# Kernel tuning notes

Hardware: AMD Instinct MI355X
Metric: run time of the kernel (lower is better)

## Reference

```python
import jax, jax.numpy as jnp
from jax import lax
import numpy as np

B, T, V, H = 512, 512, 96, 128


def setup_inputs() -> dict:
    key = jax.random.key(0)
    ks = jax.random.split(key, 8)
    # one-hot character inputs [B, T, V]
    idx = jax.random.randint(ks[0], (B, T), 0, V)
    x = jax.nn.one_hot(idx, V, dtype=jnp.float32)
    s_ih = 1.0 / np.sqrt(H)  # PyTorch nn.RNN init: U(-1/sqrt(H), 1/sqrt(H))
    W_ih = jax.random.uniform(ks[1], (H, V), jnp.float32, -s_ih, s_ih)
    b_ih = jax.random.uniform(ks[2], (H,), jnp.float32, -s_ih, s_ih)
    W_hh = jax.random.uniform(ks[3], (H, H), jnp.float32, -s_ih, s_ih)
    b_hh = jax.random.uniform(ks[4], (H,), jnp.float32, -s_ih, s_ih)
    s_fc = 1.0 / np.sqrt(H)
    W_fc = jax.random.uniform(ks[5], (V, H), jnp.float32, -s_fc, s_fc)
    b_fc = jax.random.uniform(ks[6], (V,), jnp.float32, -s_fc, s_fc)
    return {"x": x, "W_ih": W_ih, "b_ih": b_ih, "W_hh": W_hh,
            "b_hh": b_hh, "W_fc": W_fc, "b_fc": b_fc}


def reference(x, W_ih, b_ih, W_hh, b_hh, W_fc, b_fc):
    # Precompute input projection for all timesteps (batched GEMM):
    # for one-hot x this is effectively an embedding row gather.
    xW = jnp.einsum('btv,hv->bth', x, W_ih) + b_ih  # [B, T, H]

    def step(h, xt):  # h: [B, H], xt: [B, H]
        h_new = jnp.tanh(xt + h @ W_hh.T + b_hh)
        return h_new, None

    h0 = jnp.zeros((x.shape[0], W_hh.shape[0]), x.dtype)
    hT, _ = lax.scan(step, h0, jnp.swapaxes(xW, 0, 1))  # scan over T
    # fc on the last hidden state only
    return hT @ W_fc.T + b_fc  # [B, V]
```

## Files before the change

### kernel.cpp

```cpp
#include <hip/hip_runtime.h>

#define B_ 512
#define T_ 512
#define V_ 96
#define H_ 128
#define K2F 2.8853900817779268f

typedef _Float16 half8 __attribute__((ext_vector_type(8)));
typedef float    f32x4 __attribute__((ext_vector_type(4)));

__global__ __launch_bounds__(256) void onehot_idx_kernel(
    const float4* __restrict__ x4, int n4, int* __restrict__ idx)
{
    int stride = gridDim.x * blockDim.x;
    for (int e4 = blockIdx.x * blockDim.x + threadIdx.x; e4 < n4; e4 += stride) {
        float4 v = x4[e4];
        int base = e4 * 4;
        if (v.x > 0.5f) idx[(base + 0) / V_] = (base + 0) % V_;
        if (v.y > 0.5f) idx[(base + 1) / V_] = (base + 1) % V_;
        if (v.z > 0.5f) idx[(base + 2) / V_] = (base + 2) % V_;
        if (v.w > 0.5f) idx[(base + 3) / V_] = (base + 3) % V_;
    }
}

__global__ __launch_bounds__(256) void build_xwg_kernel(
    const float* __restrict__ W_ih, const float* __restrict__ b_ih,
    const float* __restrict__ b_hh, float* __restrict__ xwg)
{
    int e = blockIdx.x * 256 + threadIdx.x;
    if (e < V_ * H_) {
        int v = e >> 7, u = e & 127;
        xwg[e] = (W_ih[u * V_ + v] + b_ih[u] + b_hh[u]) * K2F;
    }
}

__global__ __launch_bounds__(256) void build_wB_kernel(
    const float* __restrict__ W_hh, _Float16* __restrict__ wB)
{
    int e = blockIdx.x * 256 + threadIdx.x;
    if (e < 16384) {
        int reg = e & 7, lane = (e >> 3) & 63, mt = (e >> 9) & 7, ks = e >> 12;
        int kin = ks * 32 + (lane >> 4) * 8 + reg;
        int m   = mt * 16 + (lane & 15);
        wB[e] = (_Float16)(K2F * W_hh[m * H_ + kin]);
    }
}

__global__ __launch_bounds__(256) void build_wBfc_kernel(
    const float* __restrict__ W_fc, _Float16* __restrict__ wBfc)
{
    int e = blockIdx.x * 256 + threadIdx.x;
    if (e < 12288) {
        int reg = e & 7, lane = (e >> 3) & 63;
        int mt = (e >> 9) % 6, ks = e / 3072;
        int kin = ks * 32 + (lane >> 4) * 8 + reg;
        int m   = mt * 16 + (lane & 15);
        wBfc[e] = (_Float16)W_fc[m * H_ + kin];
    }
}

__global__ __launch_bounds__(256, 1) void rnn_mfma4_kernel(
    const uint4* __restrict__ wBg, const uint4* __restrict__ wBfcg,
    const float* __restrict__ xwg, const int* __restrict__ idx,
    const float* __restrict__ b_fc, float* __restrict__ out)
{
    const int bb  = blockIdx.x;
    const int tid = threadIdx.x;
    const int w   = tid >> 6;
    const int l   = tid & 63;
    const int lo  = l & 15, g = l >> 4;

    __shared__ _Float16      hs[2][16][136];
    __shared__ unsigned char idxT[(T_ + 1) * 16];

    for (int e = tid; e < 16 * T_; e += 256) {
        int row = e >> 9, t = e & 511;
        idxT[t * 16 + row] = (unsigned char)idx[(bb * 16 + row) * T_ + t];
    }
    if (tid < 16) idxT[T_ * 16 + tid] = 0;
    for (int e = tid; e < 16 * 136; e += 256)
        hs[0][e / 136][e % 136] = (_Float16)0.f;

    uint4 wa[4][2];
    #pragma unroll
    for (int ks = 0; ks < 4; ++ks)
        #pragma unroll
        for (int q = 0; q < 2; ++q)
            wa[ks][q] = wBg[(ks * 8 + 2 * w + q) * 64 + l];

    __syncthreads();

    int id0 = idxT[0 * 16 + lo];
    float4 xcA = *(const float4*)(xwg + id0 * H_ + 32 * w + 4 * g);
    float4 xcB = *(const float4*)(xwg + id0 * H_ + 32 * w + 16 + 4 * g);

    int cur = 0;
    #pragma clang loop unroll(disable)
    for (int t = 0; t < T_; ++t) {
        const int idn = idxT[(t + 1) * 16 + lo];
        const float4 xnA = *(const float4*)(xwg + idn * H_ + 32 * w + 4 * g);
        const float4 xnB = *(const float4*)(xwg + idn * H_ + 32 * w + 16 + 4 * g);

        half8 bF[4];
        #pragma unroll
        for (int ks = 0; ks < 4; ++ks)
            __builtin_memcpy(&bF[ks], &hs[cur][lo][ks * 32 + g * 8], 16);

        f32x4 p0 = {xcA.x, xcA.y, xcA.z, xcA.w};
        f32x4 p1 = {xcB.x, xcB.y, xcB.z, xcB.w};
        f32x4 q0 = {0.f, 0.f, 0.f, 0.f}, q1 = {0.f, 0.f, 0.f, 0.f};
        #pragma unroll
        for (int ks = 0; ks < 2; ++ks) {
            union { uint4 u; half8 h; } u0, u1, u2, u3;
            u0.u = wa[ks][0];     u1.u = wa[ks][1];
            u2.u = wa[ks + 2][0]; u3.u = wa[ks + 2][1];
            p0 = __builtin_amdgcn_mfma_f32_16x16x32_f16(u0.h, bF[ks],     p0, 0, 0, 0);
            p1 = __builtin_amdgcn_mfma_f32_16x16x32_f16(u1.h, bF[ks],     p1, 0, 0, 0);
            q0 = __builtin_amdgcn_mfma_f32_16x16x32_f16(u2.h, bF[ks + 2], q0, 0, 0, 0);
            q1 = __builtin_amdgcn_mfma_f32_16x16x32_f16(u3.h, bF[ks + 2], q1, 0, 0, 0);
        }
        f32x4 acc0 = p0 + q0, acc1 = p1 + q1;

        _Float16 o0[4], o1[4];
        #pragma unroll
        for (int j = 0; j < 4; ++j) {
            float E0 = __builtin_amdgcn_exp2f(acc0[j]);
            float E1 = __builtin_amdgcn_exp2f(acc1[j]);
            o0[j] = (_Float16)(1.0f - 2.0f * __builtin_amdgcn_rcpf(E0 + 1.0f));
            o1[j] = (_Float16)(1.0f - 2.0f * __builtin_amdgcn_rcpf(E1 + 1.0f));
        }
        __builtin_memcpy(&hs[cur ^ 1][lo][32 * w + 4 * g], o0, 8);
        __builtin_memcpy(&hs[cur ^ 1][lo][32 * w + 16 + 4 * g], o1, 8);
        cur ^= 1;

        asm volatile("s_waitcnt lgkmcnt(0)" ::: "memory");
        __builtin_amdgcn_s_barrier();
        __builtin_amdgcn_sched_barrier(0);

        xcA = xnA; xcB = xnB;
    }

    half8 bE[4];
    #pragma unroll
    for (int ks = 0; ks < 4; ++ks)
        __builtin_memcpy(&bE[ks], &hs[0][lo][ks * 32 + g * 8], 16);
    #pragma unroll
    for (int q = 0; q < 2; ++q) {
        const int MT = 2 * w + q;
        if (MT < 6) {
            f32x4 acc;
            __builtin_memcpy(&acc, &b_fc[MT * 16 + 4 * g], 16);
            #pragma unroll
            for (int ks = 0; ks < 4; ++ks) {
                union { uint4 u; half8 h; } ua;
                ua.u = wBfcg[(ks * 6 + MT) * 64 + l];
                acc = __builtin_amdgcn_mfma_f32_16x16x32_f16(ua.h, bE[ks], acc, 0, 0, 0);
            }
            __builtin_memcpy(&out[(bb * 16 + lo) * V_ + MT * 16 + 4 * g], &acc, 16);
        }
    }
}

extern "C" void kernel_launch(void* const* d_in, const int* in_sizes, int n_in,
                              void* d_out, int out_size, void* d_ws, size_t ws_size,
                              hipStream_t stream)
{
    const float* x    = (const float*)d_in[0];
    const float* W_ih = (const float*)d_in[1];
    const float* b_ih = (const float*)d_in[2];
    const float* W_hh = (const float*)d_in[3];
    const float* b_hh = (const float*)d_in[4];
    const float* W_fc = (const float*)d_in[5];
    const float* b_fc = (const float*)d_in[6];
    float* out = (float*)d_out;

    char* ws = (char*)d_ws;
    int*      idx  = (int*)ws;
    float*    xwg  = (float*)(ws + (size_t)B_ * T_ * 4);
    _Float16* wB   = (_Float16*)((char*)xwg + V_ * H_ * 4);
    _Float16* wBfc = (_Float16*)((char*)wB + 16384 * 2);

    const int n4 = (B_ * T_ * V_) / 4;
    hipLaunchKernelGGL(onehot_idx_kernel, dim3(2048), dim3(256), 0, stream,
                       (const float4*)x, n4, idx);
    hipLaunchKernelGGL(build_xwg_kernel, dim3((V_ * H_ + 255) / 256), dim3(256),
                       0, stream, W_ih, b_ih, b_hh, xwg);
    hipLaunchKernelGGL(build_wB_kernel, dim3(64), dim3(256), 0, stream, W_hh, wB);
    hipLaunchKernelGGL(build_wBfc_kernel, dim3(48), dim3(256), 0, stream, W_fc, wBfc);
    hipLaunchKernelGGL(rnn_mfma4_kernel, dim3(B_ / 16), dim3(256), 0, stream,
                       (const uint4*)wB, (const uint4*)wBfc, xwg, idx, b_fc, out);
}
```

Measured before the change: 219.8 us.

## Fold input projection into recurrent MFMA via one-hot LDS operand

Drops the precomputed fp32 xW gather table. The input weights and both biases become three extra K-slices of the fp16 recurrent weight matrix. Each step keeps a one-hot row per sequence in a double-buffered LDS array and multiplies it with MFMA, so the per-step global gather of the input projection goes away. The cost is six extra MFMAs per wave per step, a serial one-hot update by 16 threads before the barrier, and fp16 rounding of the input term.

```diff
diff --git a/kernel.cpp b/kernel.cpp
--- a/kernel.cpp
+++ b/kernel.cpp
@@ -4,6 +4,8 @@
 #define T_ 512
 #define V_ 96
 #define H_ 128
+#define NKS 7
+#define OXP 104
 #define K2F 2.8853900817779268f
 
 typedef _Float16 half8 __attribute__((ext_vector_type(8)));
@@ -23,26 +25,23 @@
     }
 }
 
-__global__ __launch_bounds__(256) void build_xwg_kernel(
-    const float* __restrict__ W_ih, const float* __restrict__ b_ih,
-    const float* __restrict__ b_hh, float* __restrict__ xwg)
+__global__ __launch_bounds__(256) void build_wB_kernel(
+    const float* __restrict__ W_hh, const float* __restrict__ W_ih,
+    const float* __restrict__ b_ih, const float* __restrict__ b_hh,
+    _Float16* __restrict__ wB)
 {
     int e = blockIdx.x * 256 + threadIdx.x;
-    if (e < V_ * H_) {
-        int v = e >> 7, u = e & 127;
-        xwg[e] = (W_ih[u * V_ + v] + b_ih[u] + b_hh[u]) * K2F;
-    }
-}
-
-__global__ __launch_bounds__(256) void build_wB_kernel(
-    const float* __restrict__ W_hh, _Float16* __restrict__ wB)
-{
-    int e = blockIdx.x * 256 + threadIdx.x;
-    if (e < 16384) {
+    if (e < NKS * 8 * 64 * 8) {
         int reg = e & 7, lane = (e >> 3) & 63, mt = (e >> 9) & 7, ks = e >> 12;
-        int kin = ks * 32 + (lane >> 4) * 8 + reg;
-        int m   = mt * 16 + (lane & 15);
-        wB[e] = (_Float16)(K2F * W_hh[m * H_ + kin]);
+        int k = ks * 32 + ((lane >> 4) << 3) + reg;
+        int m = mt * 16 + (lane & 15);
+        float val;
+        if (k < H_) val = K2F * W_hh[m * H_ + k];
+        else {
+            int v = k - H_;
+            val = K2F * (W_ih[m * V_ + v] + b_ih[m] + b_hh[m]);
+        }
+        wB[e] = (_Float16)val;
     }
 }
 
@@ -53,7 +52,7 @@
     if (e < 12288) {
         int reg = e & 7, lane = (e >> 3) & 63;
         int mt = (e >> 9) % 6, ks = e / 3072;
-        int kin = ks * 32 + (lane >> 4) * 8 + reg;
+        int kin = ks * 32 + ((lane >> 4) << 3) + reg;
         int m   = mt * 16 + (lane & 15);
         wBfc[e] = (_Float16)W_fc[m * H_ + kin];
     }
@@ -61,8 +60,8 @@
 
 __global__ __launch_bounds__(256, 1) void rnn_mfma4_kernel(
     const uint4* __restrict__ wBg, const uint4* __restrict__ wBfcg,
-    const float* __restrict__ xwg, const int* __restrict__ idx,
-    const float* __restrict__ b_fc, float* __restrict__ out)
+    const int* __restrict__ idx, const float* __restrict__ b_fc,
+    float* __restrict__ out)
 {
     const int bb  = blockIdx.x;
     const int tid = threadIdx.x;
@@ -71,6 +70,7 @@
     const int lo  = l & 15, g = l >> 4;
 
     __shared__ _Float16      hs[2][16][136];
+    __shared__ _Float16      ox[2][16][OXP];
     __shared__ unsigned char idxT[(T_ + 1) * 16];
 
     for (int e = tid; e < 16 * T_; e += 256) {
@@ -80,35 +80,43 @@
     if (tid < 16) idxT[T_ * 16 + tid] = 0;
     for (int e = tid; e < 16 * 136; e += 256)
         hs[0][e / 136][e % 136] = (_Float16)0.f;
-
-    uint4 wa[4][2];
+    for (int e = tid; e < 2 * 16 * OXP; e += 256) {
+        int buf = e / (16 * OXP), rem = e % (16 * OXP);
+        ox[buf][rem / OXP][rem % OXP] = (_Float16)0.f;
+    }
+
+    uint4 wa[NKS][2];
     #pragma unroll
-    for (int ks = 0; ks < 4; ++ks)
+    for (int ks = 0; ks < NKS; ++ks)
         #pragma unroll
         for (int q = 0; q < 2; ++q)
             wa[ks][q] = wBg[(ks * 8 + 2 * w + q) * 64 + l];
 
     __syncthreads();
 
-    int id0 = idxT[0 * 16 + lo];
-    float4 xcA = *(const float4*)(xwg + id0 * H_ + 32 * w + 4 * g);
-    float4 xcB = *(const float4*)(xwg + id0 * H_ + 32 * w + 16 + 4 * g);
+    int idA = 0, idB = 0;
+    if (tid < 16) {
+        idA = idxT[0 * 16 + tid];
+        idB = idxT[1 * 16 + tid];
+        ox[0][tid][idA] = (_Float16)1.f;
+        ox[1][tid][idB] = (_Float16)1.f;
+    }
+    __syncthreads();
 
     int cur = 0;
     #pragma clang loop unroll(disable)
     for (int t = 0; t < T_; ++t) {
-        const int idn = idxT[(t + 1) * 16 + lo];
-        const float4 xnA = *(const float4*)(xwg + idn * H_ + 32 * w + 4 * g);
-        const float4 xnB = *(const float4*)(xwg + idn * H_ + 32 * w + 16 + 4 * g);
-
-        half8 bF[4];
+        half8 bF[NKS];
         #pragma unroll
         for (int ks = 0; ks < 4; ++ks)
             __builtin_memcpy(&bF[ks], &hs[cur][lo][ks * 32 + g * 8], 16);
-
-        f32x4 p0 = {xcA.x, xcA.y, xcA.z, xcA.w};
-        f32x4 p1 = {xcB.x, xcB.y, xcB.z, xcB.w};
-        f32x4 q0 = {0.f, 0.f, 0.f, 0.f}, q1 = {0.f, 0.f, 0.f, 0.f};
+        #pragma unroll
+        for (int ks = 4; ks < NKS; ++ks)
+            __builtin_memcpy(&bF[ks], &ox[cur][lo][(ks - 4) * 32 + g * 8], 16);
+
+        f32x4 p0 = {0.f,0.f,0.f,0.f}, p1 = {0.f,0.f,0.f,0.f};
+        f32x4 q0 = {0.f,0.f,0.f,0.f}, q1 = {0.f,0.f,0.f,0.f};
+        f32x4 r0 = {0.f,0.f,0.f,0.f}, r1 = {0.f,0.f,0.f,0.f};
         #pragma unroll
         for (int ks = 0; ks < 2; ++ks) {
             union { uint4 u; half8 h; } u0, u1, u2, u3;
@@ -119,7 +127,14 @@
             q0 = __builtin_amdgcn_mfma_f32_16x16x32_f16(u2.h, bF[ks + 2], q0, 0, 0, 0);
             q1 = __builtin_amdgcn_mfma_f32_16x16x32_f16(u3.h, bF[ks + 2], q1, 0, 0, 0);
         }
-        f32x4 acc0 = p0 + q0, acc1 = p1 + q1;
+        #pragma unroll
+        for (int ks = 4; ks < NKS; ++ks) {
+            union { uint4 u; half8 h; } u0, u1;
+            u0.u = wa[ks][0]; u1.u = wa[ks][1];
+            r0 = __builtin_amdgcn_mfma_f32_16x16x32_f16(u0.h, bF[ks], r0, 0, 0, 0);
+            r1 = __builtin_amdgcn_mfma_f32_16x16x32_f16(u1.h, bF[ks], r1, 0, 0, 0);
+        }
+        f32x4 acc0 = (p0 + q0) + r0, acc1 = (p1 + q1) + r1;
 
         _Float16 o0[4], o1[4];
         #pragma unroll
@@ -131,13 +146,16 @@
         }
         __builtin_memcpy(&hs[cur ^ 1][lo][32 * w + 4 * g], o0, 8);
         __builtin_memcpy(&hs[cur ^ 1][lo][32 * w + 16 + 4 * g], o1, 8);
+
+        if (tid < 16) {
+            const int oldid = cur ? idA : idB;
+            const int idn   = idxT[(t + 1) * 16 + tid];
+            ox[cur ^ 1][tid][oldid] = (_Float16)0.f;
+            ox[cur ^ 1][tid][idn]   = (_Float16)1.f;
+            if (cur) idA = idn; else idB = idn;
+        }
         cur ^= 1;
-
-        asm volatile("s_waitcnt lgkmcnt(0)" ::: "memory");
-        __builtin_amdgcn_s_barrier();
-        __builtin_amdgcn_sched_barrier(0);
-
-        xcA = xnA; xcB = xnB;
+        __syncthreads();
     }
 
     half8 bE[4];
@@ -176,17 +194,15 @@
 
     char* ws = (char*)d_ws;
     int*      idx  = (int*)ws;
-    float*    xwg  = (float*)(ws + (size_t)B_ * T_ * 4);
-    _Float16* wB   = (_Float16*)((char*)xwg + V_ * H_ * 4);
-    _Float16* wBfc = (_Float16*)((char*)wB + 16384 * 2);
+    _Float16* wB   = (_Float16*)(ws + (size_t)B_ * T_ * 4);
+    _Float16* wBfc = (_Float16*)((char*)wB + NKS * 8 * 64 * 8 * 2);
 
     const int n4 = (B_ * T_ * V_) / 4;
     hipLaunchKernelGGL(onehot_idx_kernel, dim3(2048), dim3(256), 0, stream,
                        (const float4*)x, n4, idx);
-    hipLaunchKernelGGL(build_xwg_kernel, dim3((V_ * H_ + 255) / 256), dim3(256),
-                       0, stream, W_ih, b_ih, b_hh, xwg);
-    hipLaunchKernelGGL(build_wB_kernel, dim3(64), dim3(256), 0, stream, W_hh, wB);
+    hipLaunchKernelGGL(build_wB_kernel, dim3((NKS * 8 * 64 * 8 + 255) / 256),
+                       dim3(256), 0, stream, W_hh, W_ih, b_ih, b_hh, wB);
     hipLaunchKernelGGL(build_wBfc_kernel, dim3(48), dim3(256), 0, stream, W_fc, wBfc);
     hipLaunchKernelGGL(rnn_mfma4_kernel, dim3(B_ / 16), dim3(256), 0, stream,
-                       (const uint4*)wB, (const uint4*)wBfc, xwg, idx, b_fc, out);
-}
+                       (const uint4*)wB, (const uint4*)wBfc, idx, b_fc, out);
+}
```

Result: slower. 249.3 us (+13.4%).
